# Kernel optimization log

Hardware: AMD Instinct MI355X
Metric: run time of the kernel (lower is better)

## Reference

```python
import jax, jax.numpy as jnp
import numpy as np

N_NODES = 50000
N_EDGES = 1200000
IN_FEATS = 64
OUT_FEATS = 64
NEG_SLOPE = 0.01  # F.leaky_relu default


def setup_inputs() -> dict:
    key = jax.random.key(0)
    k1, k2, k3, k4, k5, k6 = jax.random.split(key, 6)
    feature = jax.random.normal(k1, (N_NODES, IN_FEATS), dtype=jnp.float32)
    attn_w = jax.random.normal(k2, (2 * IN_FEATS, 1), dtype=jnp.float32) * 0.1
    lin_w = jax.random.normal(k3, (OUT_FEATS, 2 * IN_FEATS), dtype=jnp.float32) * 0.1
    lin_b = jax.random.normal(k4, (OUT_FEATS,), dtype=jnp.float32) * 0.1
    src = jax.random.randint(k5, (N_EDGES,), 0, N_NODES, dtype=jnp.int32)
    dst = jax.random.randint(k6, (N_EDGES,), 0, N_NODES, dtype=jnp.int32)
    return {"feature": feature, "attn_w": attn_w, "lin_w": lin_w,
            "lin_b": lin_b, "src": src, "dst": dst}


def reference(feature, attn_w, lin_w, lin_b, src, dst):
    N = feature.shape[0]
    # edge attention: leaky_relu(attn_fc([h_src, h_dst]))
    # split attn weight to avoid materializing the [E, 2*in] concat
    a_src, a_dst = attn_w[:IN_FEATS, 0], attn_w[IN_FEATS:, 0]
    e = jax.nn.leaky_relu(feature[src] @ a_src + feature[dst] @ a_dst,
                          negative_slope=NEG_SLOPE)  # [E]
    # segment softmax over incoming edges of each destination node
    emax = jax.ops.segment_max(e, dst, num_segments=N)
    emax = jnp.where(jnp.isfinite(emax), emax, 0.0)  # guard empty segments
    ex = jnp.exp(e - emax[dst])                       # [E]
    denom = jax.ops.segment_sum(ex, dst, num_segments=N)          # [N]
    num = jax.ops.segment_sum(ex[:, None] * feature[src], dst,
                              num_segments=N)                      # [N, in]
    hm = jnp.where(denom[:, None] > 0, num / denom[:, None], 0.0)
    # node apply: relu(Linear([h, hm]))
    h = jnp.concatenate([feature, hm], axis=1) @ lin_w.T + lin_b
    return jax.nn.relu(h)
```

## Files before the change

### kernel.cpp

```cpp
#include <hip/hip_runtime.h>
#include <math.h>

#define N_NODES 50000
#define N_EDGES 1200000
#define F 64
#define CAP 49
#define OVF_MAX 1024
#define NBIN 196
#define BSTR 16
#define CAP_BIN 7680
#define TILE 8192
#define NTILE ((N_EDGES + TILE - 1) / TILE)

typedef __attribute__((ext_vector_type(8))) short short8;
typedef __attribute__((ext_vector_type(4))) float v4f;


__device__ __forceinline__ unsigned short f32_to_bf16_rne(float f) {
    unsigned u = __float_as_uint(f);
    return (unsigned short)((u + 0x7FFFu + ((u >> 16) & 1u)) >> 16);
}

__global__ void k_prep(const float* __restrict__ feature,
                       const float* __restrict__ attn_w,
                       float* __restrict__ s, float* __restrict__ dd,
                       int* __restrict__ bin_cnt, int* __restrict__ ovf_cnt) {
    int gid = blockIdx.x * blockDim.x + threadIdx.x;
    if (gid < NBIN * BSTR) bin_cnt[gid] = 0;
    if (gid == NBIN * BSTR) *ovf_cnt = 0;
    int wave = gid >> 6;
    int lane = threadIdx.x & 63;
    if (wave >= N_NODES) return;
    float f = feature[wave * F + lane];
    float sv = f * attn_w[lane];
    float dv = f * attn_w[F + lane];
    #pragma unroll
    for (int o = 32; o > 0; o >>= 1) {
        sv += __shfl_down(sv, o, 64);
        dv += __shfl_down(dv, o, 64);
    }
    if (lane == 0) {
        s[wave] = sv;
        dd[wave] = dv;
    }
}

__global__ __launch_bounds__(256) void k_bin(
        const int* __restrict__ src, const int* __restrict__ dst,
        int* __restrict__ bin_cnt, unsigned* __restrict__ binned) {
    __shared__ unsigned ord[TILE];
    __shared__ int cnt_l[NBIN], off_l[NBIN], cur_l[NBIN], base_g[NBIN];
    __shared__ int buf[256];
    int t = threadIdx.x;
    int e0 = blockIdx.x * TILE;
    int ecnt = N_EDGES - e0; if (ecnt > TILE) ecnt = TILE;
    for (int i = t; i < NBIN; i += 256) cnt_l[i] = 0;
    __syncthreads();
    int n4 = ecnt >> 2;
    const int4* s4p = (const int4*)src + (e0 >> 2);
    const int4* d4p = (const int4*)dst + (e0 >> 2);
    for (int c = t; c < n4; c += 256) {
        int4 d4 = d4p[c];
        atomicAdd(&cnt_l[d4.x >> 8], 1);
        atomicAdd(&cnt_l[d4.y >> 8], 1);
        atomicAdd(&cnt_l[d4.z >> 8], 1);
        atomicAdd(&cnt_l[d4.w >> 8], 1);
    }
    __syncthreads();
    int v0 = (t < NBIN) ? cnt_l[t] : 0;
    buf[t] = v0;
    __syncthreads();
    #pragma unroll
    for (int d = 1; d < 256; d <<= 1) {
        int x = (t >= d) ? buf[t - d] : 0;
        __syncthreads();
        buf[t] += x;
        __syncthreads();
    }
    if (t < NBIN) {
        int off = buf[t] - v0;
        off_l[t] = off;
        cur_l[t] = off;
        base_g[t] = atomicAdd(&bin_cnt[t * BSTR], v0);
    }
    __syncthreads();
    for (int c = t; c < n4; c += 256) {
        int4 d4 = d4p[c];
        int4 s4 = s4p[c];
        int dv[4] = {d4.x, d4.y, d4.z, d4.w};
        int sv[4] = {s4.x, s4.y, s4.z, s4.w};
        #pragma unroll
        for (int u = 0; u < 4; u++) {
            int r = atomicAdd(&cur_l[dv[u] >> 8], 1);
            ord[r] = (((unsigned)dv[u]) << 16) | (unsigned)sv[u];
        }
    }
    __syncthreads();
    for (int i = t; i < ecnt; i += 256) {
        unsigned v = ord[i];
        int b = v >> 24;
        int pos = base_g[b] + (i - off_l[b]);
        if (pos < CAP_BIN) binned[(size_t)b * CAP_BIN + pos] = v;
    }
}

__global__ __launch_bounds__(256) void k_bucket(
        const unsigned* __restrict__ binned, const int* __restrict__ bin_cnt,
        int* __restrict__ cnt, unsigned short* __restrict__ bucket,
        int* __restrict__ ovf_cnt, unsigned* __restrict__ ovf) {
    __shared__ int cnt_l[256];
    __shared__ __align__(16) unsigned short buck_l[256 * CAP];
    int bin = blockIdx.x;
    int t = threadIdx.x;
    int n0 = bin << 8;
    int nn = N_NODES - n0; if (nn > 256) nn = 256;
    cnt_l[t] = 0;
    __syncthreads();
    int E = bin_cnt[bin * BSTR];
    if (E > CAP_BIN) E = CAP_BIN;
    const unsigned* be = binned + (size_t)bin * CAP_BIN;
    for (int i = t; i < E; i += 256) {
        unsigned v = be[i];
        int local = (v >> 16) & 255;
        int sid = (int)(v & 0xFFFFu);
        int r = atomicAdd(&cnt_l[local], 1);
        if (r < CAP) {
            buck_l[local * CAP + r] = (unsigned short)sid;
        } else {
            int o = atomicAdd(ovf_cnt, 1);
            if (o < OVF_MAX)
                ovf[o] = ((unsigned)(n0 + local) << 16) | (unsigned)sid;
        }
    }
    __syncthreads();
    if (t < nn) cnt[n0 + t] = cnt_l[t];
    int nu4 = (nn * CAP * 2) >> 4;
    const uint4* bl4 = (const uint4*)buck_l;
    uint4* bg4 = (uint4*)(bucket + (size_t)n0 * CAP);
    for (int i = t; i < nu4; i += 256) bg4[i] = bl4[i];
}

__global__ __launch_bounds__(512) void k_aggregate(
        const unsigned short* __restrict__ bucket,
        const int* __restrict__ cnt,
        const float* __restrict__ s, const float* __restrict__ dd,
        const float* __restrict__ feature,
        float* __restrict__ out) {
    int t = threadIdx.x;
    int wid = t >> 6, lane = t & 63;
    int n = blockIdx.x * 8 + wid;
    int deg = cnt[n];
    if (deg > CAP) return;
    if (deg == 0) { out[n * F + lane] = 0.0f; return; }
    int si = 0;
    float ev = -1e30f;
    if (lane < deg) {
        si = (int)bucket[n * CAP + lane];
        float v = s[si] + dd[n];
        ev = v > 0.0f ? v : 0.01f * v;
    }
    float m = ev;
    #pragma unroll
    for (int o = 32; o > 0; o >>= 1)
        m = fmaxf(m, __shfl_xor(m, o, 64));
    float p = (lane < deg) ? __expf(ev - m) : 0.0f;
    float l = p;
    #pragma unroll
    for (int o = 32; o > 0; o >>= 1)
        l += __shfl_xor(l, o, 64);
    p *= __builtin_amdgcn_rcpf(l);
    int half = lane >> 5;
    int col = lane & 31;
    const float2* f2 = (const float2*)feature;
    float acc0 = 0.0f, acc1 = 0.0f;
    for (int k = 0; k < deg; k += 16) {
        float2 fv[8];
        #pragma unroll
        for (int u = 0; u < 8; u++) {
            int sk = __shfl(si, k + 2 * u + half, 64);
            fv[u] = f2[sk * 32 + col];
        }
        #pragma unroll
        for (int u = 0; u < 8; u++) {
            float pw = __shfl(p, k + 2 * u + half, 64);
            acc0 = fmaf(pw, fv[u].x, acc0);
            acc1 = fmaf(pw, fv[u].y, acc1);
        }
    }
    acc0 += __shfl_xor(acc0, 32, 64);
    acc1 += __shfl_xor(acc1, 32, 64);
    if (lane < 32) {
        float2 st; st.x = acc0; st.y = acc1;
        ((float2*)out)[n * 32 + col] = st;
    }
}

__global__ __launch_bounds__(256) void k_cleanup(
        const unsigned short* __restrict__ bucket,
        const int* __restrict__ cnt,
        const int* __restrict__ ovf_cnt, const unsigned int* __restrict__ ovf,
        const float* __restrict__ s, const float* __restrict__ dd,
        const float* __restrict__ feature,
        float* __restrict__ out) {
    int M = *ovf_cnt;
    if (M > OVF_MAX) M = OVF_MAX;
    if (M == 0) return;
    __shared__ int list[128];
    __shared__ int nlist;
    __shared__ unsigned short edg[4][256];
    int t = threadIdx.x;
    if (t == 0) {
        nlist = 0;
        for (int i = 0; i < M; i++) {
            int d = (int)(ovf[i] >> 16);
            bool seen = false;
            for (int j = 0; j < nlist; j++) if (list[j] == d) seen = true;
            if (!seen && nlist < 128) list[nlist++] = d;
        }
    }
    __syncthreads();
    int wid = t >> 6, lane = t & 63;
    for (int idx = wid; idx < nlist; idx += 4) {
        int n = list[idx];
        int deg = cnt[n];
        if (lane < CAP) edg[wid][lane] = bucket[n * CAP + lane];
        int k2 = CAP;
        for (int base = 0; base < M; base += 64) {
            int i2 = base + lane;
            unsigned val = 0;
            bool mt = false;
            if (i2 < M) { val = ovf[i2]; mt = ((int)(val >> 16) == n); }
            unsigned long long mask = __ballot(mt);
            if (mt) {
                int pos = k2 + __popcll(mask & ((1ULL << lane) - 1ULL));
                if (pos < 256) edg[wid][pos] = (unsigned short)(val & 0xFFFFu);
            }
            k2 += __popcll(mask);
        }
        __threadfence_block();
        int nd = deg < 256 ? deg : 256;
        float m = -1e30f, l = 0.0f, acc = 0.0f;
        float dn = dd[n];
        for (int c0 = 0; c0 < nd; c0 += 64) {
            int j = c0 + lane;
            int sid = 0;
            float ev = -1e30f;
            if (j < nd) {
                sid = (int)edg[wid][j];
                float v = s[sid] + dn;
                ev = v > 0.0f ? v : 0.01f * v;
            }
            float cm = ev;
            #pragma unroll
            for (int o = 32; o > 0; o >>= 1)
                cm = fmaxf(cm, __shfl_xor(cm, o, 64));
            float np = (j < nd) ? __expf(ev - cm) : 0.0f;
            float cl = np;
            #pragma unroll
            for (int o = 32; o > 0; o >>= 1)
                cl += __shfl_xor(cl, o, 64);
            float cacc = 0.0f;
            int c = nd - c0; if (c > 64) c = 64;
            for (int k = 0; k < c; k += 16) {
                float fvv[16];
                #pragma unroll
                for (int u = 0; u < 16; u++) {
                    int sk = __builtin_amdgcn_readlane(sid, k + u);
                    fvv[u] = feature[sk * F + lane];
                }
                #pragma unroll
                for (int u = 0; u < 16; u++) {
                    float pk = __uint_as_float(
                        __builtin_amdgcn_readlane(__float_as_uint(np), k + u));
                    cacc = fmaf(pk, fvv[u], cacc);
                }
            }
            float mn = fmaxf(m, cm);
            float sc = __expf(m - mn);
            float sc2 = __expf(cm - mn);
            l = l * sc + cl * sc2;
            acc = acc * sc + cacc * sc2;
            m = mn;
        }
        out[n * F + lane] = acc / l;
    }
}

__global__ __launch_bounds__(256) void k_proj(
        const float* __restrict__ feature,
        const float* __restrict__ lin_w, const float* __restrict__ lin_b,
        float* __restrict__ out) {
    __shared__ unsigned short Wl[64 * 136];
    int t = threadIdx.x;
    for (int i = t; i < 64 * 128; i += 256)
        Wl[(i >> 7) * 136 + (i & 127)] = f32_to_bf16_rne(lin_w[i]);
    __syncthreads();
    int wid = t >> 6, lane = t & 63;
    int wgl = blockIdx.x * 4 + wid;
    int n0 = wgl * 16;
    if (n0 >= N_NODES) return;
    int m = lane & 15, quad = lane >> 4;
    short8 afr[4];
    #pragma unroll
    for (int ks = 0; ks < 4; ks++) {
        int kb = ks * 32 + quad * 8;
        const float* sp = (kb < 64) ? (feature + (size_t)(n0 + m) * F + kb)
                                    : (out + (size_t)(n0 + m) * F + (kb - 64));
        float4 x0 = ((const float4*)sp)[0];
        float4 x1 = ((const float4*)sp)[1];
        short8 a;
        a[0] = (short)f32_to_bf16_rne(x0.x);
        a[1] = (short)f32_to_bf16_rne(x0.y);
        a[2] = (short)f32_to_bf16_rne(x0.z);
        a[3] = (short)f32_to_bf16_rne(x0.w);
        a[4] = (short)f32_to_bf16_rne(x1.x);
        a[5] = (short)f32_to_bf16_rne(x1.y);
        a[6] = (short)f32_to_bf16_rne(x1.z);
        a[7] = (short)f32_to_bf16_rne(x1.w);
        afr[ks] = a;
    }
    #pragma unroll
    for (int nt = 0; nt < 4; nt++) {
        v4f acc = {0.0f, 0.0f, 0.0f, 0.0f};
        #pragma unroll
        for (int ks = 0; ks < 4; ks++) {
            int kb = ks * 32 + quad * 8;
            short8 b = *(const short8*)&Wl[(nt * 16 + m) * 136 + kb];
            acc = __builtin_amdgcn_mfma_f32_16x16x32_bf16(afr[ks], b, acc,
                                                          0, 0, 0);
        }
        int colo = nt * 16 + m;
        float bias = lin_b[colo];
        #pragma unroll
        for (int r = 0; r < 4; r++) {
            int row = quad * 4 + r;
            float v = acc[r] + bias;
            out[(size_t)(n0 + row) * F + colo] = fmaxf(v, 0.0f);
        }
    }
}

extern "C" void kernel_launch(void* const* d_in, const int* in_sizes, int n_in,
                              void* d_out, int out_size, void* d_ws, size_t ws_size,
                              hipStream_t stream) {
    const float* feature = (const float*)d_in[0];
    const float* attn_w  = (const float*)d_in[1];
    const float* lin_w   = (const float*)d_in[2];
    const float* lin_b   = (const float*)d_in[3];
    const int*   src     = (const int*)d_in[4];
    const int*   dst     = (const int*)d_in[5];
    float* out = (float*)d_out;
    char* ws = (char*)d_ws;

    float*          s       = (float*)(ws);
    float*          dd      = (float*)(ws + 200000);
    int*            cnt     = (int*)  (ws + 400000);
    int*            bin_cnt = (int*)  (ws + 600000);
    int*            ovf_cnt = (int*)  (ws + 612544);
    unsigned*       ovf     = (unsigned*)(ws + 612608);
    unsigned short* bucket  = (unsigned short*)(ws + 616704);
    unsigned*       binned  = (unsigned*)(ws + 5516704);

    k_prep<<<(N_NODES * 64) / 256, 256, 0, stream>>>(
        feature, attn_w, s, dd, bin_cnt, ovf_cnt);
    k_bin<<<NTILE, 256, 0, stream>>>(src, dst, bin_cnt, binned);
    k_bucket<<<NBIN, 256, 0, stream>>>(
        binned, bin_cnt, cnt, bucket, ovf_cnt, ovf);
    k_aggregate<<<N_NODES / 8, 512, 0, stream>>>(
        bucket, cnt, s, dd, feature, out);
    k_cleanup<<<1, 256, 0, stream>>>(
        bucket, cnt, ovf_cnt, ovf, s, dd, feature, out);
    k_proj<<<(3125 + 3) / 4, 256, 0, stream>>>(feature, lin_w, lin_b, out);
}
```

Measured before the change: 160.4 us.

## Gather bf16 copy of features in aggregation and reuse it in projection

The prep kernel now also writes a bf16 copy of the node features. The aggregation kernel gathers neighbour rows from that copy, using 8-byte ushort4 loads across four lane groups. It also unrolls the loop into at most two fixed 32-edge chunks instead of a 16-edge loop, and reduces with extra shuffles. The projection kernel reads its feature half directly from the bf16 copy. This halves the bytes of the random gathers but lowers the aggregation inputs to bf16 precision and adds a write pass in prep.

```diff
diff --git a/kernel.cpp b/kernel.cpp
--- a/kernel.cpp
+++ b/kernel.cpp
@@ -20,11 +20,15 @@
     unsigned u = __float_as_uint(f);
     return (unsigned short)((u + 0x7FFFu + ((u >> 16) & 1u)) >> 16);
 }
+__device__ __forceinline__ float bf16_to_f32(unsigned short u) {
+    return __uint_as_float(((unsigned)u) << 16);
+}
 
 __global__ void k_prep(const float* __restrict__ feature,
                        const float* __restrict__ attn_w,
                        float* __restrict__ s, float* __restrict__ dd,
-                       int* __restrict__ bin_cnt, int* __restrict__ ovf_cnt) {
+                       int* __restrict__ bin_cnt, int* __restrict__ ovf_cnt,
+                       unsigned short* __restrict__ fb) {
     int gid = blockIdx.x * blockDim.x + threadIdx.x;
     if (gid < NBIN * BSTR) bin_cnt[gid] = 0;
     if (gid == NBIN * BSTR) *ovf_cnt = 0;
@@ -32,6 +36,7 @@
     int lane = threadIdx.x & 63;
     if (wave >= N_NODES) return;
     float f = feature[wave * F + lane];
+    fb[wave * F + lane] = f32_to_bf16_rne(f);
     float sv = f * attn_w[lane];
     float dv = f * attn_w[F + lane];
     #pragma unroll
@@ -144,7 +149,7 @@
         const unsigned short* __restrict__ bucket,
         const int* __restrict__ cnt,
         const float* __restrict__ s, const float* __restrict__ dd,
-        const float* __restrict__ feature,
+        const unsigned short* __restrict__ fb,
         float* __restrict__ out) {
     int t = threadIdx.x;
     int wid = t >> 6, lane = t & 63;
@@ -169,29 +174,50 @@
     for (int o = 32; o > 0; o >>= 1)
         l += __shfl_xor(l, o, 64);
     p *= __builtin_amdgcn_rcpf(l);
-    int half = lane >> 5;
-    int col = lane & 31;
-    const float2* f2 = (const float2*)feature;
-    float acc0 = 0.0f, acc1 = 0.0f;
-    for (int k = 0; k < deg; k += 16) {
-        float2 fv[8];
+
+    int grp = lane >> 4;
+    int c16 = lane & 15;
+    const ushort4* f4 = (const ushort4*)fb;
+    ushort4 fv0[8], fv1[8];
+    #pragma unroll
+    for (int u = 0; u < 8; u++) {
+        int sk = __shfl(si, u * 4 + grp, 64);
+        fv0[u] = f4[sk * 16 + c16];
+    }
+    bool two = deg > 32;
+    if (two) {
         #pragma unroll
         for (int u = 0; u < 8; u++) {
-            int sk = __shfl(si, k + 2 * u + half, 64);
-            fv[u] = f2[sk * 32 + col];
-        }
+            int sk = __shfl(si, 32 + u * 4 + grp, 64);
+            fv1[u] = f4[sk * 16 + c16];
+        }
+    }
+    float a0 = 0.0f, a1 = 0.0f, a2 = 0.0f, a3 = 0.0f;
+    #pragma unroll
+    for (int u = 0; u < 8; u++) {
+        float pw = __shfl(p, u * 4 + grp, 64);
+        a0 = fmaf(pw, bf16_to_f32(fv0[u].x), a0);
+        a1 = fmaf(pw, bf16_to_f32(fv0[u].y), a1);
+        a2 = fmaf(pw, bf16_to_f32(fv0[u].z), a2);
+        a3 = fmaf(pw, bf16_to_f32(fv0[u].w), a3);
+    }
+    if (two) {
         #pragma unroll
         for (int u = 0; u < 8; u++) {
-            float pw = __shfl(p, k + 2 * u + half, 64);
-            acc0 = fmaf(pw, fv[u].x, acc0);
-            acc1 = fmaf(pw, fv[u].y, acc1);
-        }
-    }
-    acc0 += __shfl_xor(acc0, 32, 64);
-    acc1 += __shfl_xor(acc1, 32, 64);
-    if (lane < 32) {
-        float2 st; st.x = acc0; st.y = acc1;
-        ((float2*)out)[n * 32 + col] = st;
+            float pw = __shfl(p, 32 + u * 4 + grp, 64);
+            a0 = fmaf(pw, bf16_to_f32(fv1[u].x), a0);
+            a1 = fmaf(pw, bf16_to_f32(fv1[u].y), a1);
+            a2 = fmaf(pw, bf16_to_f32(fv1[u].z), a2);
+            a3 = fmaf(pw, bf16_to_f32(fv1[u].w), a3);
+        }
+    }
+    a0 += __shfl_xor(a0, 16, 64); a0 += __shfl_xor(a0, 32, 64);
+    a1 += __shfl_xor(a1, 16, 64); a1 += __shfl_xor(a1, 32, 64);
+    a2 += __shfl_xor(a2, 16, 64); a2 += __shfl_xor(a2, 32, 64);
+    a3 += __shfl_xor(a3, 16, 64); a3 += __shfl_xor(a3, 32, 64);
+    if (lane < 16) {
+        v4f st = {a0, a1, a2, a3};
+        ((v4f*)out)[n * 16 + c16] = st;
     }
 }
 
@@ -287,7 +313,7 @@
 }
 
 __global__ __launch_bounds__(256) void k_proj(
-        const float* __restrict__ feature,
+        const unsigned short* __restrict__ fb,
         const float* __restrict__ lin_w, const float* __restrict__ lin_b,
         float* __restrict__ out) {
     __shared__ unsigned short Wl[64 * 136];
@@ -302,10 +328,14 @@
     int m = lane & 15, quad = lane >> 4;
     short8 afr[4];
     #pragma unroll
-    for (int ks = 0; ks < 4; ks++) {
+    for (int ks = 0; ks < 2; ks++) {
         int kb = ks * 32 + quad * 8;
-        const float* sp = (kb < 64) ? (feature + (size_t)(n0 + m) * F + kb)
-                                    : (out + (size_t)(n0 + m) * F + (kb - 64));
+        afr[ks] = *(const short8*)&fb[(size_t)(n0 + m) * F + kb];
+    }
+    #pragma unroll
+    for (int ks = 2; ks < 4; ks++) {
+        int kb = ks * 32 + quad * 8 - 64;
+        const float* sp = out + (size_t)(n0 + m) * F + kb;
         float4 x0 = ((const float4*)sp)[0];
         float4 x1 = ((const float4*)sp)[1];
         short8 a;
@@ -360,15 +390,16 @@
     unsigned*       ovf     = (unsigned*)(ws + 612608);
     unsigned short* bucket  = (unsigned short*)(ws + 616704);
     unsigned*       binned  = (unsigned*)(ws + 5516704);
+    unsigned short* fb      = (unsigned short*)(ws + 11537824);
 
     k_prep<<<(N_NODES * 64) / 256, 256, 0, stream>>>(
-        feature, attn_w, s, dd, bin_cnt, ovf_cnt);
+        feature, attn_w, s, dd, bin_cnt, ovf_cnt, fb);
     k_bin<<<NTILE, 256, 0, stream>>>(src, dst, bin_cnt, binned);
     k_bucket<<<NBIN, 256, 0, stream>>>(
         binned, bin_cnt, cnt, bucket, ovf_cnt, ovf);
     k_aggregate<<<N_NODES / 8, 512, 0, stream>>>(
-        bucket, cnt, s, dd, feature, out);
+        bucket, cnt, s, dd, fb, out);
     k_cleanup<<<1, 256, 0, stream>>>(
         bucket, cnt, ovf_cnt, ovf, s, dd, feature, out);
-    k_proj<<<(3125 + 3) / 4, 256, 0, stream>>>(feature, lin_w, lin_b, out);
-}
+    k_proj<<<(3125 + 3) / 4, 256, 0, stream>>>(fb, lin_w, lin_b, out);
+}
```

After: 148.0 us. -7.8%, faster.
